# Optimization experiments

Measured on AMD Instinct MI355X. Metric: run time of the kernel, lower is better.

## Reference

```python
import jax, jax.numpy as jnp
import numpy as np

DIM = 1024
N_HEADS = 16
HEAD_DIM = DIM // N_HEADS  # 64
B, T = 2, 2048


def setup_inputs() -> dict:
    key = jax.random.key(0)
    k1, k2, k3, k4, k5 = jax.random.split(key, 5)
    x = jax.random.normal(k1, (B, T, DIM), dtype=jnp.float32)
    cos = jax.random.uniform(k2, (1, 1, T, HEAD_DIM // 2), dtype=jnp.float32)
    sin = jax.random.uniform(k3, (1, 1, T, HEAD_DIM // 2), dtype=jnp.float32)
    # torch Linear weights: y = x @ W.T ; qkv: [3*dim, dim], out_proj: [dim, dim]
    w_qkv = jax.random.normal(k4, (3 * DIM, DIM), dtype=jnp.float32) * 0.02
    w_out = jax.random.normal(k5, (DIM, DIM), dtype=jnp.float32) * 0.02
    return {"x": x, "cos": cos, "sin": sin, "w_qkv": w_qkv, "w_out": w_out}


def _rope(t, cos, sin):
    # t: [B, H, T, D]; cos/sin broadcast as [1,1,T,D/2]
    t1, t2 = jnp.split(t, 2, axis=-1)
    return jnp.concatenate([t1 * cos - t2 * sin, t1 * sin + t2 * cos], axis=-1)


def reference(x, cos, sin, w_qkv, w_out):
    Bb, Tt, C = x.shape
    qkv = x @ w_qkv.T                                    # [B, T, 3C]
    q, k, v = jnp.split(qkv, 3, axis=-1)
    def heads(t):
        return t.reshape(Bb, Tt, N_HEADS, HEAD_DIM).transpose(0, 2, 1, 3)
    q, k, v = heads(q), heads(k), heads(v)               # [B, H, T, D]
    q = _rope(q, cos, sin)
    k = _rope(k, cos, sin)
    scale = 1.0 / jnp.sqrt(jnp.float32(HEAD_DIM))
    scores = jnp.einsum("bhqd,bhkd->bhqk", q, k) * scale  # [B, H, T, T]
    causal = jnp.tril(jnp.ones((Tt, Tt), dtype=bool))
    scores = jnp.where(causal[None, None], scores, jnp.float32(-jnp.inf))
    attn = jax.nn.softmax(scores, axis=-1)
    out = jnp.einsum("bhqk,bhkd->bhqd", attn, v)          # [B, H, T, D]
    out = out.transpose(0, 2, 1, 3).reshape(Bb, Tt, C)
    return out @ w_out.T
```

## Files before the change

### kernel.cpp

```cpp
#include <hip/hip_runtime.h>

#define DIMC 1024
#define NH   16
#define HD   64
#define BSZ  2
#define TSZ  2048
#define MROWS (BSZ*TSZ)

typedef __attribute__((ext_vector_type(8))) short s16x8;
typedef __attribute__((ext_vector_type(4))) float f32x4;

__device__ __forceinline__ float b2f(unsigned short u) {
  return __uint_as_float(((unsigned)u) << 16);
}
__device__ __forceinline__ unsigned short f2b(float f) {
  unsigned x = __float_as_uint(f);
  unsigned r = x + 0x7fffu + ((x >> 16) & 1u);
  return (unsigned short)(r >> 16);
}
__device__ __forceinline__ unsigned pk2(float a, float b) {
  return (unsigned)f2b(a) | ((unsigned)f2b(b) << 16);
}
__device__ __forceinline__ float ldsc(const void* __restrict__ p, int idx, int isf32) {
  return isf32 ? ((const float*)p)[idx] : b2f(((const unsigned short*)p)[idx]);
}

__device__ __forceinline__ void async_cp16(const unsigned short* g, unsigned short* l) {
  __builtin_amdgcn_global_load_lds(
      (const __attribute__((address_space(1))) unsigned int*)g,
      (__attribute__((address_space(3))) unsigned int*)l, 16, 0, 0);
}

__global__ void detect_dtype(const unsigned short* __restrict__ cosp, int* __restrict__ flag) {
  const int i = threadIdx.x;
  const unsigned long long m = __ballot(cosp[i] >= 0x4000u);
  if (i == 0) *flag = (m != 0ull) ? 1 : 0;
}

__global__ __launch_bounds__(256)
void cvt_all(const float* __restrict__ x, const float* __restrict__ wq,
             const float* __restrict__ wo,
             unsigned short* __restrict__ xb, unsigned short* __restrict__ wqb,
             unsigned short* __restrict__ wob, const int* __restrict__ flag) {
  if (*flag == 0) return;
  const unsigned id = blockIdx.x * 256 + threadIdx.x;
  const float* src; unsigned short* dst; unsigned off;
  if (id < 524288u) { src = x; dst = xb; off = id; }
  else if (id < 917504u) { src = wq; dst = wqb; off = id - 524288u; }
  else { src = wo; dst = wob; off = id - 917504u; }
  const float4 a = ((const float4*)src)[off * 2];
  const float4 b = ((const float4*)src)[off * 2 + 1];
  uint4 u;
  u.x = pk2(a.x, a.y); u.y = pk2(a.z, a.w);
  u.z = pk2(b.x, b.y); u.w = pk2(b.z, b.w);
  ((uint4*)dst)[off] = u;
}

template <int EPI, int NT>
__global__ __launch_bounds__(256)
void gemm_bt_async(const void* __restrict__ Aorig, const unsigned short* __restrict__ Aconv,
                   const void* __restrict__ Worig, const unsigned short* __restrict__ Wconv,
                   void* __restrict__ C,
                   const void* __restrict__ cosp, const void* __restrict__ sinp,
                   unsigned short* __restrict__ qout,
                   unsigned short* __restrict__ kout,
                   unsigned short* __restrict__ vout,
                   const int* __restrict__ dflag, int Nsz) {
  constexpr int NJ = NT / 32;
  const int f32flag = *dflag;
  const unsigned short* A = f32flag ? Aconv : (const unsigned short*)Aorig;
  const unsigned short* W = f32flag ? Wconv : (const unsigned short*)Worig;

  const int tid = threadIdx.x;
  const int m0 = blockIdx.y * 128;
  const int n0 = blockIdx.x * NT;

  __shared__ __align__(16) unsigned short s_ab[128 * 64 + NT * 64];
  unsigned short* s_a = s_ab;
  unsigned short* s_b = s_ab + 128 * 64;

  const int lane = tid & 63;
  const int wave = tid >> 6;
  const int wm = (wave & 1) * 64;
  const int wn = (wave >> 1) * (NT / 2);
  const int m16 = lane & 15;
  const int quad = lane >> 4;

  const int srow = lane >> 3;
  const int schunk = (lane & 7) ^ srow;

  f32x4 acc[4][NJ];
#pragma unroll
  for (int i = 0; i < 4; ++i)
#pragma unroll
    for (int j = 0; j < NJ; ++j) acc[i][j] = (f32x4){0.f, 0.f, 0.f, 0.f};

  for (int kt = 0; kt < DIMC; kt += 64) {
    __syncthreads();
#pragma unroll
    for (int u = 0; u < 4; ++u) {
      const int r0 = u * 32 + wave * 8;
      async_cp16(A + (size_t)(m0 + r0 + srow) * DIMC + kt + schunk * 8, &s_a[r0 * 64]);
    }
#pragma unroll
    for (int u = 0; u < NT / 32; ++u) {
      const int r0 = u * 32 + wave * 8;
      async_cp16(W + (size_t)(n0 + r0 + srow) * DIMC + kt + schunk * 8, &s_b[r0 * 64]);
    }
    __syncthreads();
#pragma unroll
    for (int kk = 0; kk < 64; kk += 32) {
      const int cx = ((kk >> 3) + quad) ^ (m16 & 7);
      s16x8 af[4], bf[NJ];
#pragma unroll
      for (int i = 0; i < 4; ++i)
        af[i] = *(const s16x8*)&s_a[(wm + i * 16 + m16) * 64 + cx * 8];
#pragma unroll
      for (int j = 0; j < NJ; ++j)
        bf[j] = *(const s16x8*)&s_b[(wn + j * 16 + m16) * 64 + cx * 8];
#pragma unroll
      for (int i = 0; i < 4; ++i)
#pragma unroll
        for (int j = 0; j < NJ; ++j)
          acc[i][j] = __builtin_amdgcn_mfma_f32_16x16x32_bf16(af[i], bf[j], acc[i][j], 0, 0, 0);
    }
  }

  if (EPI == 1) {
    const int n_base = n0 + wn;
    const int sel = n_base >> 10;
    const int h = (n_base & 1023) >> 6;
    unsigned short* dst = (sel == 0) ? qout : ((sel == 1) ? kout : vout);
    const float qsc = (sel == 0) ? 0.125f : 1.0f;
    __syncthreads();
    unsigned short* tile = s_ab + (wave << 12);
    if (sel < 2) {
#pragma unroll
      for (int i = 0; i < 4; ++i)
#pragma unroll
        for (int r = 0; r < 4; ++r) {
          const int row_l = i * 16 + quad * 4 + r;
          const int t = (m0 + wm + row_l) & 2047;
#pragma unroll
          for (int jp = 0; jp < 2; ++jp) {
            const int d = jp * 16 + m16;
            const float c = ldsc(cosp, t * 32 + d, f32flag);
            const float sn = ldsc(sinp, t * 32 + d, f32flag);
            const float v1 = acc[i][jp][r];
            const float v2 = acc[i][jp + 2][r];
            tile[row_l * 64 + d]      = f2b((v1 * c - v2 * sn) * qsc);
            tile[row_l * 64 + d + 32] = f2b((v1 * sn + v2 * c) * qsc);
          }
        }
    } else {
#pragma unroll
      for (int i = 0; i < 4; ++i)
#pragma unroll
        for (int r = 0; r < 4; ++r) {
          const int row_l = i * 16 + quad * 4 + r;
#pragma unroll
          for (int jp = 0; jp < 4; ++jp)
            tile[row_l * 64 + jp * 16 + m16] = f2b(acc[i][jp][r]);
        }
    }
#pragma unroll
    for (int s = 0; s < 8; ++s) {
      const int row_l = s * 8 + (lane >> 3);
      const int seg = lane & 7;
      const int mrow_ = m0 + wm + row_l;
      const int bb = mrow_ >> 11;
      const int t = mrow_ & 2047;
      unsigned short* drow = dst + (((size_t)(bb * NH + h)) * TSZ + t) * HD;
      *(uint4*)(drow + seg * 8) = *(const uint4*)&tile[row_l * 64 + seg * 8];
    }
  } else {
    if (f32flag) {
      float* Cf = (float*)C;
#pragma unroll
      for (int i = 0; i < 4; ++i)
#pragma unroll
        for (int j = 0; j < NJ; ++j)
#pragma unroll
          for (int r = 0; r < 4; ++r) {
            const int mrow_ = m0 + wm + i * 16 + quad * 4 + r;
            const int col = n0 + wn + j * 16 + m16;
            Cf[(size_t)mrow_ * Nsz + col] = acc[i][j][r];
          }
    } else {
      unsigned short* Ch = (unsigned short*)C;
#pragma unroll
      for (int i = 0; i < 4; ++i)
#pragma unroll
        for (int j = 0; j < NJ; ++j)
#pragma unroll
          for (int r = 0; r < 4; ++r) {
            const int mrow_ = m0 + wm + i * 16 + quad * 4 + r;
            const int col = n0 + wn + j * 16 + m16;
            Ch[(size_t)mrow_ * Nsz + col] = f2b(acc[i][j][r]);
          }
    }
  }
}

__device__ __forceinline__ void attn_pass(
    const unsigned short* __restrict__ qgh, const unsigned short* __restrict__ kgh,
    const unsigned short* __restrict__ vgh, unsigned short* __restrict__ outg,
    int b, int h, int t, unsigned short* s_k0, unsigned short* s_k1,
    unsigned short* s_v0, unsigned short* s_v1, unsigned short* s_p,
    int tid, int lane, int w, int m16, int quad) {
  const int qs = t * 128 + w * 16;
  const unsigned short* qrow = qgh + (size_t)(qs + m16) * HD;
  const s16x8 bq0 = *(const s16x8*)(qrow + quad * 8);
  const s16x8 bq1 = *(const s16x8*)(qrow + 32 + quad * 8);

  f32x4 oacc[4];
#pragma unroll
  for (int dt = 0; dt < 4; ++dt) oacc[dt] = (f32x4){0.f, 0.f, 0.f, 0.f};
  float m_ = -1e30f, l_ = 0.f;

  const int krow = tid >> 3, kseg = tid & 7;
  const int vkey = tid & 63, vseg = tid >> 6;
  const int nc = 2 * t + 2;

  {
    const uint4 pk = *(const uint4*)(kgh + (size_t)krow * HD + kseg * 8);
    const uint4 pv = *(const uint4*)(vgh + (size_t)vkey * HD + vseg * 8);
    *(uint4*)&s_k0[krow * 72 + kseg * 8] = pk;
    const unsigned short* vv = (const unsigned short*)&pv;
#pragma unroll
    for (int jj = 0; jj < 8; ++jj) s_v0[(vseg * 8 + jj) * 72 + vkey] = vv[jj];
  }

  for (int kc = 0; kc < nc; ++kc) {
    unsigned short* sk = (kc & 1) ? s_k1 : s_k0;
    unsigned short* sv = (kc & 1) ? s_v1 : s_v0;
    unsigned short* skN = (kc & 1) ? s_k0 : s_k1;
    unsigned short* svN = (kc & 1) ? s_v0 : s_v1;
    __syncthreads();
    uint4 pk, pv;
    const int pf = (kc + 1 < nc);
    if (pf) {
      pk = *(const uint4*)(kgh + (size_t)((kc + 1) * 64 + krow) * HD + kseg * 8);
      pv = *(const uint4*)(vgh + (size_t)((kc + 1) * 64 + vkey) * HD + vseg * 8);
    }

    if (kc * 64 <= qs + 15) {
      f32x4 sacc[4];
#pragma unroll
      for (int jt = 0; jt < 4; ++jt) sacc[jt] = (f32x4){0.f, 0.f, 0.f, 0.f};
#pragma unroll
      for (int jt = 0; jt < 4; ++jt) {
        const s16x8 ak0 = *(const s16x8*)&sk[(jt * 16 + m16) * 72 + quad * 8];
        sacc[jt] = __builtin_amdgcn_mfma_f32_16x16x32_bf16(ak0, bq0, sacc[jt], 0, 0, 0);
        const s16x8 ak1 = *(const s16x8*)&sk[(jt * 16 + m16) * 72 + 32 + quad * 8];
        sacc[jt] = __builtin_amdgcn_mfma_f32_16x16x32_bf16(ak1, bq1, sacc[jt], 0, 0, 0);
      }

      if (kc * 64 + 63 > qs) {
#pragma unroll
        for (int jt = 0; jt < 4; ++jt)
#pragma unroll
          for (int r = 0; r < 4; ++r)
            if (kc * 64 + jt * 16 + quad * 4 + r > qs + m16) sacc[jt][r] = -1e30f;
      }

      float mx = sacc[0][0];
#pragma unroll
      for (int jt = 0; jt < 4; ++jt)
#pragma unroll
        for (int r = 0; r < 4; ++r) mx = fmaxf(mx, sacc[jt][r]);
      mx = fmaxf(mx, __shfl_xor(mx, 16, 64));
      mx = fmaxf(mx, __shfl_xor(mx, 32, 64));
      const float mn = fmaxf(m_, mx);
      const float alpha = __expf(m_ - mn);
      m_ = mn;
      float rs = 0.f;
#pragma unroll
      for (int jt = 0; jt < 4; ++jt)
#pragma unroll
        for (int r = 0; r < 4; ++r) {
          const float p = __expf(sacc[jt][r] - mn);
          sacc[jt][r] = p;
          rs += p;
        }
      rs += __shfl_xor(rs, 16, 64);
      rs += __shfl_xor(rs, 32, 64);
      l_ = l_ * alpha + rs;
#pragma unroll
      for (int dt = 0; dt < 4; ++dt)
#pragma unroll
        for (int r = 0; r < 4; ++r) oacc[dt][r] *= alpha;

#pragma unroll
      for (int jt = 0; jt < 4; ++jt) {
        uint2 pw;
        pw.x = pk2(sacc[jt][0], sacc[jt][1]);
        pw.y = pk2(sacc[jt][2], sacc[jt][3]);
        *(uint2*)&s_p[(w * 16 + m16) * 72 + jt * 16 + quad * 4] = pw;
      }

#pragma unroll
      for (int kk = 0; kk < 64; kk += 32) {
        const s16x8 bp = *(const s16x8*)&s_p[(w * 16 + m16) * 72 + kk + quad * 8];
#pragma unroll
        for (int dt = 0; dt < 4; ++dt) {
          const s16x8 av = *(const s16x8*)&sv[(dt * 16 + m16) * 72 + kk + quad * 8];
          oacc[dt] = __builtin_amdgcn_mfma_f32_16x16x32_bf16(av, bp, oacc[dt], 0, 0, 0);
        }
      }
    }

    if (pf) {
      *(uint4*)&skN[krow * 72 + kseg * 8] = pk;
      const unsigned short* vv = (const unsigned short*)&pv;
#pragma unroll
      for (int jj = 0; jj < 8; ++jj) svN[(vseg * 8 + jj) * 72 + vkey] = vv[jj];
    }
  }

  const float linv = 1.0f / l_;
#pragma unroll
  for (int dt = 0; dt < 4; ++dt) {
    uint2 ow;
    ow.x = pk2(oacc[dt][0] * linv, oacc[dt][1] * linv);
    ow.y = pk2(oacc[dt][2] * linv, oacc[dt][3] * linv);
    *(uint2*)&s_p[(w * 16 + m16) * 72 + dt * 16 + quad * 4] = ow;
  }
  {
    const int qq = lane >> 2, dseg = lane & 3;
    const uint4 o0 = *(const uint4*)&s_p[(w * 16 + qq) * 72 + dseg * 16];
    const uint4 o1 = *(const uint4*)&s_p[(w * 16 + qq) * 72 + dseg * 16 + 8];
    unsigned short* orow =
        outg + ((size_t)b * TSZ + qs + qq) * DIMC + h * 64 + dseg * 16;
    *(uint4*)orow = o0;
    *(uint4*)(orow + 8) = o1;
  }
}

__global__ __launch_bounds__(512)
void attn_fwd_mfma(const unsigned short* __restrict__ qg,
                   const unsigned short* __restrict__ kg,
                   const unsigned short* __restrict__ vg,
                   unsigned short* __restrict__ outg) {
  const int tid = threadIdx.x;
  const int lane = tid & 63;
  const int w = tid >> 6;
  const int m16 = lane & 15;
  const int quad = lane >> 4;
  const int bh = (int)blockIdx.x >> 3;
  const int p = (int)blockIdx.x & 7;
  const int b = bh >> 4, h = bh & 15;
  const size_t base = (size_t)bh * TSZ * HD;

  __shared__ __align__(16) unsigned short s_k0[64 * 72];
  __shared__ __align__(16) unsigned short s_k1[64 * 72];
  __shared__ __align__(16) unsigned short s_v0[64 * 72];
  __shared__ __align__(16) unsigned short s_v1[64 * 72];
  __shared__ __align__(16) unsigned short s_p[128 * 72];

  attn_pass(qg + base, kg + base, vg + base, outg, b, h, 15 - p,
            s_k0, s_k1, s_v0, s_v1, s_p, tid, lane, w, m16, quad);
  attn_pass(qg + base, kg + base, vg + base, outg, b, h, p,
            s_k0, s_k1, s_v0, s_v1, s_p, tid, lane, w, m16, quad);
}

extern "C" void kernel_launch(void* const* d_in, const int* in_sizes, int n_in,
                              void* d_out, int out_size, void* d_ws, size_t ws_size,
                              hipStream_t stream) {
  (void)in_sizes; (void)n_in; (void)out_size; (void)ws_size;
  const void* x    = d_in[0];
  const void* cosp = d_in[1];
  const void* sinp = d_in[2];
  const void* wqkv = d_in[3];
  const void* wout = d_in[4];

  int* dflag = (int*)d_ws;
  const size_t per = (size_t)BSZ * NH * TSZ * HD;
  unsigned short* q = (unsigned short*)((char*)d_ws + 256);
  unsigned short* k = q + per;
  unsigned short* v = k + per;
  unsigned short* attnb = v + per;
  unsigned short* xb   = attnb + (size_t)MROWS * DIMC;
  unsigned short* wqb  = xb + (size_t)MROWS * DIMC;
  unsigned short* wob  = wqb + (size_t)3 * DIMC * DIMC;

  detect_dtype<<<1, 64, 0, stream>>>((const unsigned short*)cosp, dflag);
  cvt_all<<<dim3(4096), dim3(256), 0, stream>>>(
      (const float*)x, (const float*)wqkv, (const float*)wout, xb, wqb, wob, dflag);
  gemm_bt_async<1, 128><<<dim3(3 * DIMC / 128, MROWS / 128), dim3(256), 0, stream>>>(
      x, xb, wqkv, wqb, nullptr, cosp, sinp, q, k, v, dflag, 3 * DIMC);
  attn_fwd_mfma<<<dim3(256), dim3(512), 0, stream>>>(q, k, v, attnb);
  gemm_bt_async<0, 64><<<dim3(DIMC / 64, MROWS / 128), dim3(256), 0, stream>>>(
      attnb, attnb, wout, wob, d_out, nullptr, nullptr,
      nullptr, nullptr, nullptr, dflag, DIMC);
}
```

Before: 208.0 us.

## Split attention into one q-tile per block and use 128x64 GEMM tiles

The QKV GEMM now uses 128x64 output tiles with four waves each covering 32 rows, which doubles the grid to 1536 blocks and changes the per-wave epilogue tile layout. The attention kernel launches 512 blocks, each handling one query tile, instead of 256 blocks that each processed a heavy and a light tile in sequence. Heaviest tiles are scheduled first via the blockIdx mapping. Both changes aim to increase parallelism and CU occupancy on the 256-CU part, at the cost of more B-tile reloads in the GEMM and less balanced per-block work in attention.

```diff
diff --git a/kernel.cpp b/kernel.cpp
--- a/kernel.cpp
+++ b/kernel.cpp
@@ -56,7 +56,7 @@
   ((uint4*)dst)[off] = u;
 }
 
-template <int EPI, int NT>
+template <int EPI>
 __global__ __launch_bounds__(256)
 void gemm_bt_async(const void* __restrict__ Aorig, const unsigned short* __restrict__ Aconv,
                    const void* __restrict__ Worig, const unsigned short* __restrict__ Wconv,
@@ -66,34 +66,32 @@
                    unsigned short* __restrict__ kout,
                    unsigned short* __restrict__ vout,
                    const int* __restrict__ dflag, int Nsz) {
-  constexpr int NJ = NT / 32;
   const int f32flag = *dflag;
   const unsigned short* A = f32flag ? Aconv : (const unsigned short*)Aorig;
   const unsigned short* W = f32flag ? Wconv : (const unsigned short*)Worig;
 
   const int tid = threadIdx.x;
   const int m0 = blockIdx.y * 128;
-  const int n0 = blockIdx.x * NT;
-
-  __shared__ __align__(16) unsigned short s_ab[128 * 64 + NT * 64];
+  const int n0 = blockIdx.x * 64;
+
+  __shared__ __align__(16) unsigned short s_ab[128 * 64 + 64 * 64];
   unsigned short* s_a = s_ab;
   unsigned short* s_b = s_ab + 128 * 64;
 
   const int lane = tid & 63;
   const int wave = tid >> 6;
-  const int wm = (wave & 1) * 64;
-  const int wn = (wave >> 1) * (NT / 2);
+  const int wm = wave * 32;
   const int m16 = lane & 15;
   const int quad = lane >> 4;
 
   const int srow = lane >> 3;
   const int schunk = (lane & 7) ^ srow;
 
-  f32x4 acc[4][NJ];
-#pragma unroll
-  for (int i = 0; i < 4; ++i)
-#pragma unroll
-    for (int j = 0; j < NJ; ++j) acc[i][j] = (f32x4){0.f, 0.f, 0.f, 0.f};
+  f32x4 acc[2][4];
+#pragma unroll
+  for (int i = 0; i < 2; ++i)
+#pragma unroll
+    for (int j = 0; j < 4; ++j) acc[i][j] = (f32x4){0.f, 0.f, 0.f, 0.f};
 
   for (int kt = 0; kt < DIMC; kt += 64) {
     __syncthreads();
@@ -103,7 +101,7 @@
       async_cp16(A + (size_t)(m0 + r0 + srow) * DIMC + kt + schunk * 8, &s_a[r0 * 64]);
     }
 #pragma unroll
-    for (int u = 0; u < NT / 32; ++u) {
+    for (int u = 0; u < 2; ++u) {
       const int r0 = u * 32 + wave * 8;
       async_cp16(W + (size_t)(n0 + r0 + srow) * DIMC + kt + schunk * 8, &s_b[r0 * 64]);
     }
@@ -111,32 +109,31 @@
 #pragma unroll
     for (int kk = 0; kk < 64; kk += 32) {
       const int cx = ((kk >> 3) + quad) ^ (m16 & 7);
-      s16x8 af[4], bf[NJ];
-#pragma unroll
-      for (int i = 0; i < 4; ++i)
+      s16x8 af[2], bf[4];
+#pragma unroll
+      for (int i = 0; i < 2; ++i)
         af[i] = *(const s16x8*)&s_a[(wm + i * 16 + m16) * 64 + cx * 8];
 #pragma unroll
-      for (int j = 0; j < NJ; ++j)
-        bf[j] = *(const s16x8*)&s_b[(wn + j * 16 + m16) * 64 + cx * 8];
-#pragma unroll
-      for (int i = 0; i < 4; ++i)
-#pragma unroll
-        for (int j = 0; j < NJ; ++j)
+      for (int j = 0; j < 4; ++j)
+        bf[j] = *(const s16x8*)&s_b[(j * 16 + m16) * 64 + cx * 8];
+#pragma unroll
+      for (int i = 0; i < 2; ++i)
+#pragma unroll
+        for (int j = 0; j < 4; ++j)
           acc[i][j] = __builtin_amdgcn_mfma_f32_16x16x32_bf16(af[i], bf[j], acc[i][j], 0, 0, 0);
     }
   }
 
   if (EPI == 1) {
-    const int n_base = n0 + wn;
-    const int sel = n_base >> 10;
-    const int h = (n_base & 1023) >> 6;
+    const int sel = n0 >> 10;
+    const int h = (n0 & 1023) >> 6;
     unsigned short* dst = (sel == 0) ? qout : ((sel == 1) ? kout : vout);
     const float qsc = (sel == 0) ? 0.125f : 1.0f;
     __syncthreads();
-    unsigned short* tile = s_ab + (wave << 12);
+    unsigned short* tile = s_ab + wave * 2048;
     if (sel < 2) {
 #pragma unroll
-      for (int i = 0; i < 4; ++i)
+      for (int i = 0; i < 2; ++i)
 #pragma unroll
         for (int r = 0; r < 4; ++r) {
           const int row_l = i * 16 + quad * 4 + r;
@@ -154,7 +151,7 @@
         }
     } else {
 #pragma unroll
-      for (int i = 0; i < 4; ++i)
+      for (int i = 0; i < 2; ++i)
 #pragma unroll
         for (int r = 0; r < 4; ++r) {
           const int row_l = i * 16 + quad * 4 + r;
@@ -164,7 +161,7 @@
         }
     }
 #pragma unroll
-    for (int s = 0; s < 8; ++s) {
+    for (int s = 0; s < 4; ++s) {
       const int row_l = s * 8 + (lane >> 3);
       const int seg = lane & 7;
       const int mrow_ = m0 + wm + row_l;
@@ -177,25 +174,25 @@
     if (f32flag) {
       float* Cf = (float*)C;
 #pragma unroll
-      for (int i = 0; i < 4; ++i)
-#pragma unroll
-        for (int j = 0; j < NJ; ++j)
+      for (int i = 0; i < 2; ++i)
+#pragma unroll
+        for (int j = 0; j < 4; ++j)
 #pragma unroll
           for (int r = 0; r < 4; ++r) {
             const int mrow_ = m0 + wm + i * 16 + quad * 4 + r;
-            const int col = n0 + wn + j * 16 + m16;
+            const int col = n0 + j * 16 + m16;
             Cf[(size_t)mrow_ * Nsz + col] = acc[i][j][r];
           }
     } else {
       unsigned short* Ch = (unsigned short*)C;
 #pragma unroll
-      for (int i = 0; i < 4; ++i)
-#pragma unroll
-        for (int j = 0; j < NJ; ++j)
+      for (int i = 0; i < 2; ++i)
+#pragma unroll
+        for (int j = 0; j < 4; ++j)
 #pragma unroll
           for (int r = 0; r < 4; ++r) {
             const int mrow_ = m0 + wm + i * 16 + quad * 4 + r;
-            const int col = n0 + wn + j * 16 + m16;
+            const int col = n0 + j * 16 + m16;
             Ch[(size_t)mrow_ * Nsz + col] = f2b(acc[i][j][r]);
           }
     }
@@ -347,8 +344,9 @@
   const int w = tid >> 6;
   const int m16 = lane & 15;
   const int quad = lane >> 4;
-  const int bh = (int)blockIdx.x >> 3;
-  const int p = (int)blockIdx.x & 7;
+  const int l = (int)blockIdx.x;
+  const int t = 15 - (l >> 5);
+  const int bh = l & 31;
   const int b = bh >> 4, h = bh & 15;
   const size_t base = (size_t)bh * TSZ * HD;
 
@@ -358,9 +356,7 @@
   __shared__ __align__(16) unsigned short s_v1[64 * 72];
   __shared__ __align__(16) unsigned short s_p[128 * 72];
 
-  attn_pass(qg + base, kg + base, vg + base, outg, b, h, 15 - p,
-            s_k0, s_k1, s_v0, s_v1, s_p, tid, lane, w, m16, quad);
-  attn_pass(qg + base, kg + base, vg + base, outg, b, h, p,
+  attn_pass(qg + base, kg + base, vg + base, outg, b, h, t,
             s_k0, s_k1, s_v0, s_v1, s_p, tid, lane, w, m16, quad);
 }
 
@@ -387,10 +383,10 @@
   detect_dtype<<<1, 64, 0, stream>>>((const unsigned short*)cosp, dflag);
   cvt_all<<<dim3(4096), dim3(256), 0, stream>>>(
       (const float*)x, (const float*)wqkv, (const float*)wout, xb, wqb, wob, dflag);
-  gemm_bt_async<1, 128><<<dim3(3 * DIMC / 128, MROWS / 128), dim3(256), 0, stream>>>(
+  gemm_bt_async<1><<<dim3(3 * DIMC / 64, MROWS / 128), dim3(256), 0, stream>>>(
       x, xb, wqkv, wqb, nullptr, cosp, sinp, q, k, v, dflag, 3 * DIMC);
-  attn_fwd_mfma<<<dim3(256), dim3(512), 0, stream>>>(q, k, v, attnb);
-  gemm_bt_async<0, 64><<<dim3(DIMC / 64, MROWS / 128), dim3(256), 0, stream>>>(
+  attn_fwd_mfma<<<dim3(512), dim3(512), 0, stream>>>(q, k, v, attnb);
+  gemm_bt_async<0><<<dim3(DIMC / 64, MROWS / 128), dim3(256), 0, stream>>>(
       attnb, attnb, wout, wob, d_out, nullptr, nullptr,
       nullptr, nullptr, nullptr, dflag, DIMC);
 }
```

New measurement: 195.2 us. 1.07x faster.
